# Kernel optimization log

Hardware: AMD Instinct MI355X
Metric: run time of the kernel (lower is better)

Reference implementation:

```python
import jax, jax.numpy as jnp
import numpy as np

LN_EPS = 1e-3  # Keras LayerNormalization default epsilon
EPS = 1e-8     # slot-attention weight epsilon
NUM_ITERS = 3


def layer_norm(x, g, b):
    m = jnp.mean(x, axis=-1, keepdims=True)
    v = jnp.var(x, axis=-1, keepdims=True)
    return g * (x - m) * jax.lax.rsqrt(v + LN_EPS) + b


def gru_cell(x, h, Wx, Wh, b_in, b_rec):
    # Keras GRUCell (reset_after=True): separate input and recurrent biases
    gx = x @ Wx + b_in      # [K, 3D]
    gh = h @ Wh + b_rec     # [K, 3D]
    xz, xr, xh = jnp.split(gx, 3, axis=-1)
    hz, hr, hh = jnp.split(gh, 3, axis=-1)
    z = jax.nn.sigmoid(xz + hz)
    r = jax.nn.sigmoid(xr + hr)
    h_cand = jnp.tanh(xh + r * hh)
    return z * h + (1.0 - z) * h_cand


def setup_inputs() -> dict:
    key = jax.random.key(0)
    N, C, D, H, K = 262144, 64, 64, 128, 4
    ks = jax.random.split(key, 32)
    w = lambda k, s: (jax.random.normal(k, s, jnp.float32) * 0.02)
    inp = {
        "x": jax.random.normal(ks[0], (N, C), jnp.float32),
        "noise_fg": jax.random.normal(ks[1], (K - 1, D), jnp.float32),
        "noise_bg": jax.random.normal(ks[2], (1, D), jnp.float32),
        "ln_in_g": jnp.ones((C,), jnp.float32),
        "ln_in_b": jnp.zeros((C,), jnp.float32),
        "mu_fg": w(ks[3], (1, D)),
        "log_sigma_fg": w(ks[4], (1, D)),
        "mu_bg": w(ks[5], (1, D)),
        "log_sigma_bg": w(ks[6], (1, D)),
        "Wk": w(ks[7], (C, D)),
        "Wv": w(ks[8], (C, D)),
        "qfg_g": jnp.ones((D,), jnp.float32),
        "qfg_b": jnp.zeros((D,), jnp.float32),
        "Wq_fg": w(ks[9], (D, D)),
        "qbg_g": jnp.ones((D,), jnp.float32),
        "qbg_b": jnp.zeros((D,), jnp.float32),
        "Wq_bg": w(ks[10], (D, D)),
        "gru_fg_Wx": w(ks[11], (D, 3 * D)),
        "gru_fg_Wh": w(ks[12], (D, 3 * D)),
        "gru_fg_bin": jnp.zeros((3 * D,), jnp.float32),
        "gru_fg_brec": jnp.zeros((3 * D,), jnp.float32),
        "gru_bg_Wx": w(ks[13], (D, 3 * D)),
        "gru_bg_Wh": w(ks[14], (D, 3 * D)),
        "gru_bg_bin": jnp.zeros((3 * D,), jnp.float32),
        "gru_bg_brec": jnp.zeros((3 * D,), jnp.float32),
        "mfg_g": jnp.ones((D,), jnp.float32),
        "mfg_b": jnp.zeros((D,), jnp.float32),
        "mfg_W1": w(ks[15], (D, H)),
        "mfg_b1": jnp.zeros((H,), jnp.float32),
        "mfg_W2": w(ks[16], (H, D)),
        "mfg_b2": jnp.zeros((D,), jnp.float32),
        "mbg_g": jnp.ones((D,), jnp.float32),
        "mbg_b": jnp.zeros((D,), jnp.float32),
        "mbg_W1": w(ks[17], (D, H)),
        "mbg_b1": jnp.zeros((H,), jnp.float32),
        "mbg_W2": w(ks[18], (H, D)),
        "mbg_b2": jnp.zeros((D,), jnp.float32),
    }
    return inp


def reference(x, noise_fg, noise_bg, ln_in_g, ln_in_b, mu_fg, log_sigma_fg, mu_bg,
              log_sigma_bg, Wk, Wv, qfg_g, qfg_b, Wq_fg, qbg_g, qbg_b, Wq_bg,
              gru_fg_Wx, gru_fg_Wh, gru_fg_bin, gru_fg_brec,
              gru_bg_Wx, gru_bg_Wh, gru_bg_bin, gru_bg_brec,
              mfg_g, mfg_b, mfg_W1, mfg_b1, mfg_W2, mfg_b2,
              mbg_g, mbg_b, mbg_W1, mbg_b1, mbg_W2, mbg_b2):
    D = Wk.shape[1]
    scale = D ** (-0.5)
    x = layer_norm(x, ln_in_g, ln_in_b)
    k = x @ Wk  # [N, D]
    v = x @ Wv  # [N, D]
    slots_fg = mu_fg + jnp.exp(log_sigma_fg) * noise_fg  # [K-1, D]
    slots_bg = mu_bg + jnp.exp(log_sigma_bg) * noise_bg  # [1, D]
    attn = None
    for _ in range(NUM_ITERS):
        q_fg = layer_norm(slots_fg, qfg_g, qfg_b) @ Wq_fg * scale  # [K-1, D]
        q_bg = layer_norm(slots_bg, qbg_g, qbg_b) @ Wq_bg * scale  # [1, D]
        logits = jnp.concatenate([k @ q_bg.T, k @ q_fg.T], axis=-1)  # [N, K]
        attn = jax.nn.softmax(logits, axis=-1)  # competition over slots
        w_all = attn + EPS
        w_all = w_all / jnp.sum(w_all, axis=0, keepdims=True)  # normalize over N
        updates = w_all.T @ v  # [K, D]
        upd_bg, upd_fg = updates[:1], updates[1:]
        slots_bg = gru_cell(upd_bg, slots_bg, gru_bg_Wx, gru_bg_Wh, gru_bg_bin, gru_bg_brec)
        slots_fg = gru_cell(upd_fg, slots_fg, gru_fg_Wx, gru_fg_Wh, gru_fg_bin, gru_fg_brec)
        h_bg = jax.nn.relu(layer_norm(slots_bg, mbg_g, mbg_b) @ mbg_W1 + mbg_b1)
        slots_bg = slots_bg + h_bg @ mbg_W2 + mbg_b2
        h_fg = jax.nn.relu(layer_norm(slots_fg, mfg_g, mfg_b) @ mfg_W1 + mfg_b1)
        slots_fg = slots_fg + h_fg @ mfg_W2 + mfg_b2
    slots = jnp.concatenate([slots_bg, slots_fg], axis=0)  # [K, D]
    return slots, attn.T  # attn: [K, N]
```

## Files before the change

kernel.cpp:

```cpp
#include <hip/hip_runtime.h>
#include <hip/hip_bf16.h>

#define N_ROWS   262144
#define ATT_BLOCKS 512
#define CHUNKS   2
#define LN_EPS_F 1e-3f
#define EPS_W    1e-8f
#define NEPS_F   (262144.0f*1e-8f)

__device__ __forceinline__ float bf2f(unsigned u){ return __uint_as_float((u&0xffffu)<<16); }
__device__ __forceinline__ unsigned cvtpk(float lo, float hi){
  unsigned r;
  asm("v_cvt_pk_bf16_f32 %0, %1, %2" : "=v"(r) : "v"(lo), "v"(hi));
  return r;
}
__device__ __forceinline__ float wave_sum64(float v){
#pragma unroll
  for (int off=1; off<64; off<<=1) v += __shfl_xor(v, off);
  return v;
}

__global__ __launch_bounds__(256) void attn_pass_kernel(
    const float* __restrict__ x, uint* __restrict__ xhat,
    const float* __restrict__ ucoef, float* __restrict__ pT,
    float* __restrict__ attn_out, float* __restrict__ slots,
    const float* __restrict__ noise_fg, const float* __restrict__ noise_bg,
    const float* __restrict__ mu_fg, const float* __restrict__ ls_fg,
    const float* __restrict__ mu_bg, const float* __restrict__ ls_bg,
    const float* __restrict__ ln_g, const float* __restrict__ ln_b,
    const float* __restrict__ Wk,
    const float* __restrict__ qfg_g, const float* __restrict__ qfg_b, const float* __restrict__ Wq_fg,
    const float* __restrict__ qbg_g, const float* __restrict__ qbg_b, const float* __restrict__ Wq_bg,
    int first, int last)
{
  __shared__ __align__(16) ushort xs[64*256];
  __shared__ __align__(16) uint2 attn_s[256];
  __shared__ __align__(16) float qs[256];
  __shared__ float qc[4];
  __shared__ float l4[256], q4s[256];
  const int tid = threadIdx.x;
  const int w = tid>>6, ln = tid&63;
  const int lm = ln&15, lg = ln>>4;
  const int blk = blockIdx.x;

  if (first){
    const float h0 = (w==0) ? fmaf(expf(ls_bg[ln]), noise_bg[ln], mu_bg[ln])
                            : fmaf(expf(ls_fg[ln]), noise_fg[(w-1)*64+ln], mu_fg[ln]);
    if (blk == 0) slots[w*64+ln] = h0;
    const float m  = wave_sum64(h0) * (1.f/64.f);
    const float vr = wave_sum64((h0-m)*(h0-m)) * (1.f/64.f);
    const float rs = rsqrtf(vr + LN_EPS_F);
    l4[tid] = (w==0?qbg_g:qfg_g)[ln]*(h0-m)*rs + (w==0?qbg_b:qfg_b)[ln];
    __syncthreads();
    {
      const float* __restrict__ Wqj = (w==0) ? Wq_bg : Wq_fg;
      float acc = 0.f;
#pragma unroll
      for (int dd = 0; dd < 64; ++dd) acc = fmaf(l4[w*64+dd], Wqj[dd*64+ln], acc);
      q4s[tid] = acc * 0.125f;
    }
    __syncthreads();
    {
      float t = 0.f;
#pragma unroll
      for (int oo = 0; oo < 64; ++oo) t = fmaf(Wk[ln*64+oo], q4s[w*64+oo], t);
      qs[ln*4 + w] = ln_g[ln]*t;
      const float cc = wave_sum64(ln_b[ln]*t);
      if (ln == 0) qc[w] = cc;
    }
  } else {
    qs[tid] = ucoef[tid];
    if (tid < 4) qc[tid] = ucoef[256+tid];
  }
  __syncthreads();

  float n0=0.f,n1=0.f,n2=0.f,n3=0.f, vs=0.f;
  float cs0=0.f, cs1=0.f, cs2=0.f, cs3=0.f;

  auto compute_chunk = [&](int c){
    const size_t rg = (size_t)blk*(CHUNKS*256) + (size_t)c*256;
    const int lrow = w*64 + lm*4;
    float la[4][4] = {};
#pragma unroll
    for (int dd = 0; dd < 16; ++dd){
      const int d = lg*16 + dd;
      const uint2 kk = *(const uint2*)&xs[d*256 + (((lrow>>3) ^ ((d*5)&31))<<3) + (lrow&7)];
      const float e0 = bf2f(kk.x), e1 = bf2f(kk.x>>16);
      const float e2 = bf2f(kk.y), e3 = bf2f(kk.y>>16);
      const float4 q4 = *(const float4*)&qs[d*4];
#pragma unroll
      for (int s = 0; s < 4; ++s){
        const float qv = (s==0)?q4.x:(s==1)?q4.y:(s==2)?q4.z:q4.w;
        la[0][s] = fmaf(e0, qv, la[0][s]);
        la[1][s] = fmaf(e1, qv, la[1][s]);
        la[2][s] = fmaf(e2, qv, la[2][s]);
        la[3][s] = fmaf(e3, qv, la[3][s]);
      }
    }
#pragma unroll
    for (int r = 0; r < 4; ++r)
#pragma unroll
      for (int s = 0; s < 4; ++s){
        la[r][s] += __shfl_xor(la[r][s], 16);
        la[r][s] += __shfl_xor(la[r][s], 32);
        la[r][s] += qc[s];
      }
    float av[4][4];
#pragma unroll
    for (int r = 0; r < 4; ++r){
      const float mx = fmaxf(fmaxf(la[r][0],la[r][1]), fmaxf(la[r][2],la[r][3]));
      const float e0 = __expf(la[r][0]-mx), e1 = __expf(la[r][1]-mx);
      const float e2 = __expf(la[r][2]-mx), e3 = __expf(la[r][3]-mx);
      const float inv = 1.0f/((e0+e1)+(e2+e3));
      av[r][0]=e0*inv; av[r][1]=e1*inv; av[r][2]=e2*inv; av[r][3]=e3*inv;
      cs0 += av[r][0]; cs1 += av[r][1]; cs2 += av[r][2]; cs3 += av[r][3];
    }
    if (lg == 0){
#pragma unroll
      for (int r = 0; r < 4; ++r){
        uint2 pk;
        pk.x = cvtpk(av[r][0], av[r][1]);
        pk.y = cvtpk(av[r][2], av[r][3]);
        attn_s[lrow + r] = pk;
      }
      if (last){
#pragma unroll
        for (int s = 0; s < 4; ++s){
          float4 o; o.x=av[0][s]; o.y=av[1][s]; o.z=av[2][s]; o.w=av[3][s];
          *(float4*)&attn_out[(size_t)s*N_ROWS + rg + lrow] = o;
        }
      }
    }
#pragma unroll
    for (int rb = 0; rb < 8; ++rb){
      const int ch = w*8 + rb;
      const uint4 vv = *(const uint4*)&xs[ln*256 + ((ch ^ ((ln*5)&31))<<3)];
      const ushort* vp = (const ushort*)&vv;
#pragma unroll
      for (int k2 = 0; k2 < 8; ++k2){
        const uint2 au = attn_s[ch*8 + k2];
        const float b0 = bf2f(au.x), b1 = bf2f(au.x>>16);
        const float b2 = bf2f(au.y), b3 = bf2f(au.y>>16);
        const float vvv = bf2f((unsigned)vp[k2]);
        n0 = fmaf(b0, vvv, n0); n1 = fmaf(b1, vvv, n1);
        n2 = fmaf(b2, vvv, n2); n3 = fmaf(b3, vvv, n3);
        vs += vvv;
      }
    }
  };

  if (first){
    for (int c = 0; c < CHUNKS; ++c){
      const size_t rg = (size_t)blk*(CHUNKS*256) + (size_t)c*256;
#pragma unroll
      for (int mi = 0; mi < 4; ++mi){
        const int trow = w*64 + mi*16 + lm;
        const float* xr = &x[(rg + trow)*64 + lg*8];
        const float4 a0 = *(const float4*)xr;
        const float4 a1 = *(const float4*)(xr+4);
        const float4 b0 = *(const float4*)(xr+32);
        const float4 b1 = *(const float4*)(xr+36);
        float s1 = ((a0.x+a0.y)+(a0.z+a0.w)) + ((a1.x+a1.y)+(a1.z+a1.w))
                 + ((b0.x+b0.y)+(b0.z+b0.w)) + ((b1.x+b1.y)+(b1.z+b1.w));
        float s2 = a0.x*a0.x; s2=fmaf(a0.y,a0.y,s2); s2=fmaf(a0.z,a0.z,s2); s2=fmaf(a0.w,a0.w,s2);
        s2=fmaf(a1.x,a1.x,s2); s2=fmaf(a1.y,a1.y,s2); s2=fmaf(a1.z,a1.z,s2); s2=fmaf(a1.w,a1.w,s2);
        s2=fmaf(b0.x,b0.x,s2); s2=fmaf(b0.y,b0.y,s2); s2=fmaf(b0.z,b0.z,s2); s2=fmaf(b0.w,b0.w,s2);
        s2=fmaf(b1.x,b1.x,s2); s2=fmaf(b1.y,b1.y,s2); s2=fmaf(b1.z,b1.z,s2); s2=fmaf(b1.w,b1.w,s2);
        s1 += __shfl_xor(s1,16); s2 += __shfl_xor(s2,16);
        s1 += __shfl_xor(s1,32); s2 += __shfl_xor(s2,32);
        const float m  = s1*(1.0f/64.0f);
        const float rs = rsqrtf(s2*(1.0f/64.0f) - m*m + LN_EPS_F);
        const float nm = -m*rs;
        float xv[16];
        xv[0]=fmaf(a0.x,rs,nm); xv[1]=fmaf(a0.y,rs,nm); xv[2]=fmaf(a0.z,rs,nm); xv[3]=fmaf(a0.w,rs,nm);
        xv[4]=fmaf(a1.x,rs,nm); xv[5]=fmaf(a1.y,rs,nm); xv[6]=fmaf(a1.z,rs,nm); xv[7]=fmaf(a1.w,rs,nm);
        xv[8]=fmaf(b0.x,rs,nm); xv[9]=fmaf(b0.y,rs,nm); xv[10]=fmaf(b0.z,rs,nm); xv[11]=fmaf(b0.w,rs,nm);
        xv[12]=fmaf(b1.x,rs,nm); xv[13]=fmaf(b1.y,rs,nm); xv[14]=fmaf(b1.z,rs,nm); xv[15]=fmaf(b1.w,rs,nm);
        const int ch = trow>>3, rr2 = trow&7;
#pragma unroll
        for (int p = 0; p < 8; ++p){
          const int d = lg*8 + p;
          xs[d*256 + ((ch ^ ((d*5)&31))<<3) + rr2] = (ushort)cvtpk(xv[p], xv[p]);
        }
#pragma unroll
        for (int p = 0; p < 8; ++p){
          const int d = 32 + lg*8 + p;
          xs[d*256 + ((ch ^ ((d*5)&31))<<3) + rr2] = (ushort)cvtpk(xv[8+p], xv[8+p]);
        }
      }
      __syncthreads();
      const size_t tile = (size_t)(blk*CHUNKS + c);
#pragma unroll
      for (int k = 0; k < 8; ++k){
        const int i = k*256 + tid;
        *(uint4*)&xhat[tile*8192 + i*4] = *(const uint4*)&xs[i*8];
      }
      compute_chunk(c);
      __syncthreads();
    }
  } else {
    uint4 sv[8];
    {
      const size_t t0 = (size_t)blk*CHUNKS;
#pragma unroll
      for (int k = 0; k < 8; ++k){ const int i = k*256 + tid; sv[k] = *(const uint4*)&xhat[t0*8192 + i*4]; }
#pragma unroll
      for (int k = 0; k < 8; ++k){ const int i = k*256 + tid; *(uint4*)&xs[i*8] = sv[k]; }
      __syncthreads();
    }
    for (int c = 0; c < CHUNKS; ++c){
      if (c+1 < CHUNKS){
        const size_t tl = (size_t)(blk*CHUNKS + c + 1);
#pragma unroll
        for (int k = 0; k < 8; ++k){ const int i = k*256 + tid; sv[k] = *(const uint4*)&xhat[tl*8192 + i*4]; }
      }
      compute_chunk(c);
      __syncthreads();
      if (c+1 < CHUNKS){
#pragma unroll
        for (int k = 0; k < 8; ++k){ const int i = k*256 + tid; *(uint4*)&xs[i*8] = sv[k]; }
        __syncthreads();
      }
    }
  }

  cs0 = wave_sum64(cs0)*0.25f; cs1 = wave_sum64(cs1)*0.25f;
  cs2 = wave_sum64(cs2)*0.25f; cs3 = wave_sum64(cs3)*0.25f;
  float* fp = (float*)xs;
  fp[w*256 + 0*64 + ln] = n0;
  fp[w*256 + 1*64 + ln] = n1;
  fp[w*256 + 2*64 + ln] = n2;
  fp[w*256 + 3*64 + ln] = n3;
  fp[1024 + w*64 + ln] = vs;
  if (ln == 0){ fp[1280+w*4+0]=cs0; fp[1280+w*4+1]=cs1; fp[1280+w*4+2]=cs2; fp[1280+w*4+3]=cs3; }
  __syncthreads();
  float* pb = pT + (size_t)blk*324;
  pb[tid] = fp[tid] + fp[256+tid] + fp[512+tid] + fp[768+tid];
  if (tid < 64)
    pb[256 + tid] = fp[1024+tid] + fp[1088+tid] + fp[1152+tid] + fp[1216+tid];
  if (tid < 4)
    pb[320 + tid] = fp[1280+tid] + fp[1284+tid] + fp[1288+tid] + fp[1292+tid];
}

__global__ __launch_bounds__(512) void update_kernel(int mode,
    const float* __restrict__ pT,
    float* __restrict__ slots, float* __restrict__ ucoef, float* __restrict__ out,
    const float* __restrict__ ln_g, const float* __restrict__ ln_b,
    const float* __restrict__ Wk, const float* __restrict__ Wv,
    const float* __restrict__ qfg_g, const float* __restrict__ qfg_b, const float* __restrict__ Wq_fg,
    const float* __restrict__ qbg_g, const float* __restrict__ qbg_b, const float* __restrict__ Wq_bg,
    const float* __restrict__ gfWx, const float* __restrict__ gfWh,
    const float* __restrict__ gfbin, const float* __restrict__ gfbrec,
    const float* __restrict__ gbWx, const float* __restrict__ gbWh,
    const float* __restrict__ gbbin, const float* __restrict__ gbbrec,
    const float* __restrict__ mfg_g, const float* __restrict__ mfg_b,
    const float* __restrict__ mfW1, const float* __restrict__ mfb1,
    const float* __restrict__ mfW2, const float* __restrict__ mfb2,
    const float* __restrict__ mbg_g, const float* __restrict__ mbg_b,
    const float* __restrict__ mbW1, const float* __restrict__ mbb1,
    const float* __restrict__ mbW2, const float* __restrict__ mbb2)
{
  const int j = blockIdx.x;
  const int tid = threadIdx.x;
  const int ln = tid & 63, wv = tid >> 6;
  const bool bg = (j == 0);

  __shared__ __align__(16) float wlds[24640];
  __shared__ float bi_s[192], br_s[192], b1_s[128], b2_s[64];
  __shared__ float mg_s[64], mbv_s[64], qg_s[64], qb_s[64], gl_s[64], bl_s[64];
  __shared__ float vin_s[64], u_s[64], h_s[64], hg_s[64], l_s[64], h1_s[128], ql_s[64];
  __shared__ float gxp[2][192], ghp[2][192];
  __shared__ float pn_s[8][64], pv_s[8][64], csw[8];
  __shared__ float p4[4][128], p8[8][64];

  const float* __restrict__ Wx = bg?gbWx:gfWx;  const float* __restrict__ Wh = bg?gbWh:gfWh;
  const float* __restrict__ bi = bg?gbbin:gfbin; const float* __restrict__ br = bg?gbbrec:gfbrec;
  const float* __restrict__ W1 = bg?mbW1:mfW1;  const float* __restrict__ b1 = bg?mbb1:mfb1;
  const float* __restrict__ W2 = bg?mbW2:mfW2;  const float* __restrict__ b2 = bg?mbb2:mfb2;
  const float* __restrict__ Wq = bg?Wq_bg:Wq_fg;

  float hnew = 0.f;

  if (tid < 192){ bi_s[tid] = bi[tid]; br_s[tid] = br[tid]; }
  else if (tid < 320){ const int i2 = tid-192; b1_s[i2] = b1[i2]; }
  else if (tid < 384){ const int i2 = tid-320; b2_s[i2] = b2[i2]; }
  else if (tid < 448){ const int i2 = tid-384; mg_s[i2] = (bg?mbg_g:mfg_g)[i2]; mbv_s[i2] = (bg?mbg_b:mfg_b)[i2]; }
  else               { const int i2 = tid-448; qg_s[i2] = (bg?qbg_g:qfg_g)[i2]; qb_s[i2] = (bg?qbg_b:qfg_b)[i2]; }
  if (tid < 64){ gl_s[tid] = ln_g[tid]; bl_s[tid] = ln_b[tid]; }
  { const float4* sA = (const float4*)Wx; const float4* sB = (const float4*)Wh;
    float4* dA = (float4*)wlds; float4* dB = (float4*)(wlds + 12288);
#pragma unroll
    for (int i = 0; i < 6; ++i){ dA[tid + i*512] = sA[tid + i*512]; dB[tid + i*512] = sB[tid + i*512]; } }

  {
    float a0 = 0.f, a1 = 0.f, a2 = 0.f;
    float c0 = 0.f, c1v = 0.f, c2v = 0.f;
    for (int bb = 0; bb < ATT_BLOCKS/8; bb += 16){
#pragma unroll
      for (int u = 0; u < 16; u += 2){
        const float* pa = pT + (size_t)((bb+u  )*8 + wv)*324;
        const float* pc = pT + (size_t)((bb+u+1)*8 + wv)*324;
        a0 += pa[j*64 + ln];  a1 += pa[256 + ln];  a2 += pa[320 + j];
        c0 += pc[j*64 + ln];  c1v += pc[256 + ln]; c2v += pc[320 + j];
      }
    }
    pn_s[wv][ln] = a0 + c0; pv_s[wv][ln] = a1 + c1v;
    if (ln == 0) csw[wv] = a2 + c2v;
  }
  if (tid < 64) h_s[tid] = slots[j*64 + tid];
  __syncthreads();
  if (tid < 64) {
    const float csum = ((csw[0]+csw[1])+(csw[2]+csw[3])) + ((csw[4]+csw[5])+(csw[6]+csw[7])) + NEPS_F;
    float nm = 0.f, vm = 0.f;
#pragma unroll
    for (int p2 = 0; p2 < 8; ++p2){ nm += pn_s[p2][tid]; vm += pv_s[p2][tid]; }
    vin_s[tid] = gl_s[tid]*(nm + EPS_W*vm)/csum + bl_s[tid];
  }
  __syncthreads();
  { const int p8i = tid >> 6;
    float a = 0.f;
    float wbuf[8];
#pragma unroll
    for (int dd = 0; dd < 8; ++dd) wbuf[dd] = Wv[(p8i*8+dd)*64 + ln];
#pragma unroll
    for (int dd = 0; dd < 8; ++dd) a = fmaf(vin_s[p8i*8+dd], wbuf[dd], a);
    p8[p8i][ln] = a;
  }
  __syncthreads();
  if (tid < 64)
    u_s[tid] = ((p8[0][tid]+p8[1][tid])+(p8[2][tid]+p8[3][tid]))
             + ((p8[4][tid]+p8[5][tid])+(p8[6][tid]+p8[7][tid]));
  __syncthreads();
  if (tid < 384) {
    const int gcol = tid % 192, gp = tid / 192;
    float ax = 0.f, ah = 0.f;
#pragma unroll
    for (int dd = 0; dd < 32; ++dd) {
      ax = fmaf(u_s[gp*32+dd], wlds[(gp*32+dd)*192 + gcol], ax);
      ah = fmaf(h_s[gp*32+dd], wlds[12288 + (gp*32+dd)*192 + gcol], ah);
    }
    gxp[gp][gcol] = ax; ghp[gp][gcol] = ah;
  }
  __syncthreads();
  { const float4* s1 = (const float4*)W1; const float4* s2 = (const float4*)W2; const float4* s3 = (const float4*)Wq;
    float4* d1 = (float4*)wlds; float4* d2 = (float4*)(wlds + 8192); float4* d3 = (float4*)(wlds + 16384);
#pragma unroll
    for (int i = 0; i < 4; ++i){ d1[tid + i*512] = s1[tid + i*512]; d2[tid + i*512] = s2[tid + i*512]; }
#pragma unroll
    for (int i = 0; i < 2; ++i){ d3[tid + i*512] = s3[tid + i*512]; }
#pragma unroll
    for (int k = 0; k < 8; ++k){
      const int i = tid + k*512;
      wlds[20480 + (i&63)*65 + (i>>6)] = Wk[i];
    } }
  if (tid < 64) {
    const float gx0 = gxp[0][tid]     + gxp[1][tid]     + bi_s[tid];
    const float gh0 = ghp[0][tid]     + ghp[1][tid]     + br_s[tid];
    const float gx1 = gxp[0][64+tid]  + gxp[1][64+tid]  + bi_s[64+tid];
    const float gh1 = ghp[0][64+tid]  + ghp[1][64+tid]  + br_s[64+tid];
    const float gx2 = gxp[0][128+tid] + gxp[1][128+tid] + bi_s[128+tid];
    const float gh2 = ghp[0][128+tid] + ghp[1][128+tid] + br_s[128+tid];
    const float h  = h_s[tid];
    const float z  = 1.f/(1.f + expf(-(gx0 + gh0)));
    const float rr = 1.f/(1.f + expf(-(gx1 + gh1)));
    const float hc = tanhf(gx2 + rr*gh2);
    const float hg = z*h + (1.f - z)*hc;
    hg_s[tid] = hg;
    const float m  = wave_sum64(hg) * (1.f/64.f);
    const float vr = wave_sum64((hg-m)*(hg-m)) * (1.f/64.f);
    const float rs = rsqrtf(vr + LN_EPS_F);
    l_s[tid] = mg_s[tid]*(hg-m)*rs + mbv_s[tid];
  }
  __syncthreads();
  { const int p4i = tid >> 7, hi = tid & 127;
    float a = 0.f;
#pragma unroll
    for (int dd = 0; dd < 16; ++dd) a = fmaf(l_s[p4i*16+dd], wlds[(p4i*16+dd)*128 + hi], a);
    p4[p4i][hi] = a;
  }
  __syncthreads();
  if (tid < 128) h1_s[tid] = fmaxf(((p4[0][tid]+p4[1][tid])+(p4[2][tid]+p4[3][tid])) + b1_s[tid], 0.f);
  __syncthreads();
  { const int p8i = tid >> 6;
    float a = 0.f;
#pragma unroll
    for (int dd = 0; dd < 16; ++dd) a = fmaf(h1_s[p8i*16+dd], wlds[8192 + (p8i*16+dd)*64 + ln], a);
    p8[p8i][ln] = a;
  }
  __syncthreads();
  if (tid < 64) {
    hnew = hg_s[tid] + b2_s[tid]
         + ((p8[0][tid]+p8[1][tid])+(p8[2][tid]+p8[3][tid]))
         + ((p8[4][tid]+p8[5][tid])+(p8[6][tid]+p8[7][tid]));
    slots[j*64 + tid] = hnew;
  }

  if (mode == 3) {
    if (tid < 64) out[j*64 + tid] = hnew;
  } else {
    if (tid < 64) {
      const float m  = wave_sum64(hnew) * (1.f/64.f);
      const float vr = wave_sum64((hnew-m)*(hnew-m)) * (1.f/64.f);
      const float rs = rsqrtf(vr + LN_EPS_F);
      l_s[tid] = qg_s[tid]*(hnew-m)*rs + qb_s[tid];
    }
    __syncthreads();
    { const int p8i = tid >> 6;
      float a = 0.f;
#pragma unroll
      for (int dd = 0; dd < 8; ++dd) a = fmaf(l_s[p8i*8+dd], wlds[16384 + (p8i*8+dd)*64 + ln], a);
      p8[p8i][ln] = a;
    }
    __syncthreads();
    if (tid < 64)
      ql_s[tid] = (((p8[0][tid]+p8[1][tid])+(p8[2][tid]+p8[3][tid]))
                  +((p8[4][tid]+p8[5][tid])+(p8[6][tid]+p8[7][tid]))) * 0.125f;
    __syncthreads();
    if (tid < 256){
      const int d = tid & 63, pt = tid >> 6;
      float ts = 0.f;
#pragma unroll
      for (int oo = 0; oo < 16; ++oo){
        const int o = pt*16 + oo;
        ts = fmaf(wlds[20480 + o*65 + d], ql_s[o], ts);
      }
      p8[pt][d] = ts;
    }
    __syncthreads();
    if (tid < 64){
      const float t = (p8[0][tid]+p8[1][tid]) + (p8[2][tid]+p8[3][tid]);
      ucoef[tid*4 + j] = gl_s[tid]*t;
      const float c = wave_sum64(bl_s[tid]*t);
      if (tid == 0) ucoef[256 + j] = c;
    }
  }
}

extern "C" void kernel_launch(void* const* d_in, const int* in_sizes, int n_in,
                              void* d_out, int out_size, void* d_ws, size_t ws_size,
                              hipStream_t stream)
{
  const float* x        = (const float*)d_in[0];
  const float* noise_fg = (const float*)d_in[1];
  const float* noise_bg = (const float*)d_in[2];
  const float* ln_g     = (const float*)d_in[3];
  const float* ln_b     = (const float*)d_in[4];
  const float* mu_fg    = (const float*)d_in[5];
  const float* ls_fg    = (const float*)d_in[6];
  const float* mu_bg    = (const float*)d_in[7];
  const float* ls_bg    = (const float*)d_in[8];
  const float* Wk       = (const float*)d_in[9];
  const float* Wv       = (const float*)d_in[10];
  const float* qfg_g    = (const float*)d_in[11];
  const float* qfg_b    = (const float*)d_in[12];
  const float* Wq_fg    = (const float*)d_in[13];
  const float* qbg_g    = (const float*)d_in[14];
  const float* qbg_b    = (const float*)d_in[15];
  const float* Wq_bg    = (const float*)d_in[16];
  const float* gfWx     = (const float*)d_in[17];
  const float* gfWh     = (const float*)d_in[18];
  const float* gfbin    = (const float*)d_in[19];
  const float* gfbrec   = (const float*)d_in[20];
  const float* gbWx     = (const float*)d_in[21];
  const float* gbWh     = (const float*)d_in[22];
  const float* gbbin    = (const float*)d_in[23];
  const float* gbbrec   = (const float*)d_in[24];
  const float* mfg_g    = (const float*)d_in[25];
  const float* mfg_b    = (const float*)d_in[26];
  const float* mfW1     = (const float*)d_in[27];
  const float* mfb1     = (const float*)d_in[28];
  const float* mfW2     = (const float*)d_in[29];
  const float* mfb2     = (const float*)d_in[30];
  const float* mbg_g    = (const float*)d_in[31];
  const float* mbg_b    = (const float*)d_in[32];
  const float* mbW1     = (const float*)d_in[33];
  const float* mbb1     = (const float*)d_in[34];
  const float* mbW2     = (const float*)d_in[35];
  const float* mbb2     = (const float*)d_in[36];

  float* out = (float*)d_out;

  char* ws = (char*)d_ws;
  uint*  xhat  = (uint*)ws;
  float* fws   = (float*)(ws + (size_t)ATT_BLOCKS*CHUNKS*8192*4);
  float* slots = fws;
  float* ucoef = fws + 256;
  float* pT    = fws + 1024;
  float* attn_out = out + 256;

  auto launch_attn = [&](int first, int last){
    attn_pass_kernel<<<ATT_BLOCKS, 256, 0, stream>>>(x, xhat, ucoef, pT, attn_out, slots,
      noise_fg, noise_bg, mu_fg, ls_fg, mu_bg, ls_bg, ln_g, ln_b, Wk,
      qfg_g, qfg_b, Wq_fg, qbg_g, qbg_b, Wq_bg, first, last);
  };
  auto launch_update = [&](int mode){
    update_kernel<<<4, 512, 0, stream>>>(mode, pT, slots, ucoef, out,
      ln_g, ln_b, Wk, Wv,
      qfg_g, qfg_b, Wq_fg, qbg_g, qbg_b, Wq_bg,
      gfWx, gfWh, gfbin, gfbrec, gbWx, gbWh, gbbin, gbbrec,
      mfg_g, mfg_b, mfW1, mfb1, mfW2, mfb2,
      mbg_g, mbg_b, mbW1, mbb1, mbW2, mbb2);
  };

  launch_attn(1, 0);
  launch_update(1);
  launch_attn(0, 0);
  launch_update(2);
  launch_attn(0, 1);
  launch_update(3);
}
```

Baseline: 109.4 us.

## Fuse slot update into attention pass via last-block atomic tail reduction

Removes the separate update kernel. The last four blocks of each attention pass detect completion through an atomic counter, spin until every block has arrived, then each computes one slot's GRU/MLP update and the next query coefficients. This cuts three kernel launches and their gaps. In exchange the update reads weights straight from global memory instead of staging them in LDS, it adds a spin-wait, and it needs a memset of the counters on each call.

```diff
diff --git a/kernel.cpp b/kernel.cpp
--- a/kernel.cpp
+++ b/kernel.cpp
@@ -22,31 +22,44 @@
 
 __global__ __launch_bounds__(256) void attn_pass_kernel(
     const float* __restrict__ x, uint* __restrict__ xhat,
-    const float* __restrict__ ucoef, float* __restrict__ pT,
-    float* __restrict__ attn_out, float* __restrict__ slots,
+    float* __restrict__ ucoef, float* __restrict__ pT,
+    float* __restrict__ attn_out, float* __restrict__ slots, float* __restrict__ out_slots,
+    int* __restrict__ cnt,
     const float* __restrict__ noise_fg, const float* __restrict__ noise_bg,
     const float* __restrict__ mu_fg, const float* __restrict__ ls_fg,
     const float* __restrict__ mu_bg, const float* __restrict__ ls_bg,
     const float* __restrict__ ln_g, const float* __restrict__ ln_b,
-    const float* __restrict__ Wk,
+    const float* __restrict__ Wk, const float* __restrict__ Wv,
     const float* __restrict__ qfg_g, const float* __restrict__ qfg_b, const float* __restrict__ Wq_fg,
     const float* __restrict__ qbg_g, const float* __restrict__ qbg_b, const float* __restrict__ Wq_bg,
-    int first, int last)
+    const float* __restrict__ gfWx, const float* __restrict__ gfWh,
+    const float* __restrict__ gfbin, const float* __restrict__ gfbrec,
+    const float* __restrict__ gbWx, const float* __restrict__ gbWh,
+    const float* __restrict__ gbbin, const float* __restrict__ gbbrec,
+    const float* __restrict__ mfg_g, const float* __restrict__ mfg_b,
+    const float* __restrict__ mfW1, const float* __restrict__ mfb1,
+    const float* __restrict__ mfW2, const float* __restrict__ mfb2,
+    const float* __restrict__ mbg_g, const float* __restrict__ mbg_b,
+    const float* __restrict__ mbW1, const float* __restrict__ mbb1,
+    const float* __restrict__ mbW2, const float* __restrict__ mbb2,
+    int pass)
 {
   __shared__ __align__(16) ushort xs[64*256];
   __shared__ __align__(16) uint2 attn_s[256];
   __shared__ __align__(16) float qs[256];
   __shared__ float qc[4];
-  __shared__ float l4[256], q4s[256];
+  __shared__ float l4[256], q4s[256], slot0_s[256];
+  __shared__ int tailj_s;
   const int tid = threadIdx.x;
   const int w = tid>>6, ln = tid&63;
   const int lm = ln&15, lg = ln>>4;
   const int blk = blockIdx.x;
+  const int first = (pass == 0), last = (pass == 2);
 
   if (first){
     const float h0 = (w==0) ? fmaf(expf(ls_bg[ln]), noise_bg[ln], mu_bg[ln])
                             : fmaf(expf(ls_fg[ln]), noise_fg[(w-1)*64+ln], mu_fg[ln]);
-    if (blk == 0) slots[w*64+ln] = h0;
+    slot0_s[tid] = h0;
     const float m  = wave_sum64(h0) * (1.f/64.f);
     const float vr = wave_sum64((h0-m)*(h0-m)) * (1.f/64.f);
     const float rs = rsqrtf(vr + LN_EPS_F);
@@ -240,126 +253,116 @@
     pb[256 + tid] = fp[1024+tid] + fp[1088+tid] + fp[1152+tid] + fp[1216+tid];
   if (tid < 4)
     pb[320 + tid] = fp[1280+tid] + fp[1284+tid] + fp[1288+tid] + fp[1292+tid];
-}
-
-__global__ __launch_bounds__(512) void update_kernel(int mode,
-    const float* __restrict__ pT,
-    float* __restrict__ slots, float* __restrict__ ucoef, float* __restrict__ out,
-    const float* __restrict__ ln_g, const float* __restrict__ ln_b,
-    const float* __restrict__ Wk, const float* __restrict__ Wv,
-    const float* __restrict__ qfg_g, const float* __restrict__ qfg_b, const float* __restrict__ Wq_fg,
-    const float* __restrict__ qbg_g, const float* __restrict__ qbg_b, const float* __restrict__ Wq_bg,
-    const float* __restrict__ gfWx, const float* __restrict__ gfWh,
-    const float* __restrict__ gfbin, const float* __restrict__ gfbrec,
-    const float* __restrict__ gbWx, const float* __restrict__ gbWh,
-    const float* __restrict__ gbbin, const float* __restrict__ gbbrec,
-    const float* __restrict__ mfg_g, const float* __restrict__ mfg_b,
-    const float* __restrict__ mfW1, const float* __restrict__ mfb1,
-    const float* __restrict__ mfW2, const float* __restrict__ mfb2,
-    const float* __restrict__ mbg_g, const float* __restrict__ mbg_b,
-    const float* __restrict__ mbW1, const float* __restrict__ mbb1,
-    const float* __restrict__ mbW2, const float* __restrict__ mbb2)
-{
-  const int j = blockIdx.x;
-  const int tid = threadIdx.x;
-  const int ln = tid & 63, wv = tid >> 6;
-  const bool bg = (j == 0);
-
-  __shared__ __align__(16) float wlds[24640];
-  __shared__ float bi_s[192], br_s[192], b1_s[128], b2_s[64];
-  __shared__ float mg_s[64], mbv_s[64], qg_s[64], qb_s[64], gl_s[64], bl_s[64];
-  __shared__ float vin_s[64], u_s[64], h_s[64], hg_s[64], l_s[64], h1_s[128], ql_s[64];
-  __shared__ float gxp[2][192], ghp[2][192];
-  __shared__ float pn_s[8][64], pv_s[8][64], csw[8];
-  __shared__ float p4[4][128], p8[8][64];
-
-  const float* __restrict__ Wx = bg?gbWx:gfWx;  const float* __restrict__ Wh = bg?gbWh:gfWh;
-  const float* __restrict__ bi = bg?gbbin:gfbin; const float* __restrict__ br = bg?gbbrec:gfbrec;
-  const float* __restrict__ W1 = bg?mbW1:mfW1;  const float* __restrict__ b1 = bg?mbb1:mfb1;
-  const float* __restrict__ W2 = bg?mbW2:mfW2;  const float* __restrict__ b2 = bg?mbb2:mfb2;
-  const float* __restrict__ Wq = bg?Wq_bg:Wq_fg;
-
-  float hnew = 0.f;
-
-  if (tid < 192){ bi_s[tid] = bi[tid]; br_s[tid] = br[tid]; }
-  else if (tid < 320){ const int i2 = tid-192; b1_s[i2] = b1[i2]; }
-  else if (tid < 384){ const int i2 = tid-320; b2_s[i2] = b2[i2]; }
-  else if (tid < 448){ const int i2 = tid-384; mg_s[i2] = (bg?mbg_g:mfg_g)[i2]; mbv_s[i2] = (bg?mbg_b:mfg_b)[i2]; }
-  else               { const int i2 = tid-448; qg_s[i2] = (bg?qbg_g:qfg_g)[i2]; qb_s[i2] = (bg?qbg_b:qfg_b)[i2]; }
-  if (tid < 64){ gl_s[tid] = ln_g[tid]; bl_s[tid] = ln_b[tid]; }
-  { const float4* sA = (const float4*)Wx; const float4* sB = (const float4*)Wh;
-    float4* dA = (float4*)wlds; float4* dB = (float4*)(wlds + 12288);
-#pragma unroll
-    for (int i = 0; i < 6; ++i){ dA[tid + i*512] = sA[tid + i*512]; dB[tid + i*512] = sB[tid + i*512]; } }
+
+  __threadfence();
+  if (tid == 0){
+    const int old = atomicAdd(&cnt[pass], 1);
+    tailj_s = (old >= ATT_BLOCKS-4) ? (old - (ATT_BLOCKS-4)) : -1;
+  }
+  __syncthreads();
+  const int tj = tailj_s;
+  if (tj < 0) return;
+  if (tid == 0){ while (atomicAdd(&cnt[pass], 0) < ATT_BLOCKS) {} }
+  __syncthreads();
+  __threadfence();
+
+  const bool bg = (tj == 0);
+  const float* __restrict__ Wxp = bg?gbWx:gfWx;  const float* __restrict__ Whp = bg?gbWh:gfWh;
+  const float* __restrict__ bip = bg?gbbin:gfbin; const float* __restrict__ brp = bg?gbbrec:gfbrec;
+  const float* __restrict__ W1p = bg?mbW1:mfW1;  const float* __restrict__ b1p = bg?mbb1:mfb1;
+  const float* __restrict__ W2p = bg?mbW2:mfW2;  const float* __restrict__ b2p = bg?mbb2:mfb2;
+  const float* __restrict__ Wqp = bg?Wq_bg:Wq_fg;
+  const float* __restrict__ Wvp = Wv;
+
+  float* fx = (float*)xs;
+  float* pn4 = fx;
+  float* pv4 = fx + 256;
+  float* cs4 = fx + 512;
+  float* vin_s = fx + 520;
+  float* u_s   = fx + 584;
+  float* h_s   = fx + 648;
+  float* gx_s  = fx + 720;
+  float* gh_s  = fx + 912;
+  float* hg_s  = fx + 1104;
+  float* l_s2  = fx + 1168;
+  float* h1_s  = fx + 1232;
+  float* pu    = fx + 1360;
+  float* pm    = fx + 1616;
+  float* ql2   = fx + 1872;
 
   {
-    float a0 = 0.f, a1 = 0.f, a2 = 0.f;
-    float c0 = 0.f, c1v = 0.f, c2v = 0.f;
-    for (int bb = 0; bb < ATT_BLOCKS/8; bb += 16){
+    float a0=0,a1=0,a2=0, c0=0,c1=0,c2=0;
+    for (int bb = 0; bb < ATT_BLOCKS/4; bb += 16){
 #pragma unroll
       for (int u = 0; u < 16; u += 2){
-        const float* pa = pT + (size_t)((bb+u  )*8 + wv)*324;
-        const float* pc = pT + (size_t)((bb+u+1)*8 + wv)*324;
-        a0 += pa[j*64 + ln];  a1 += pa[256 + ln];  a2 += pa[320 + j];
-        c0 += pc[j*64 + ln];  c1v += pc[256 + ln]; c2v += pc[320 + j];
-      }
-    }
-    pn_s[wv][ln] = a0 + c0; pv_s[wv][ln] = a1 + c1v;
-    if (ln == 0) csw[wv] = a2 + c2v;
-  }
-  if (tid < 64) h_s[tid] = slots[j*64 + tid];
-  __syncthreads();
-  if (tid < 64) {
-    const float csum = ((csw[0]+csw[1])+(csw[2]+csw[3])) + ((csw[4]+csw[5])+(csw[6]+csw[7])) + NEPS_F;
+        const float* pa = pT + (size_t)((bb+u  )*4 + w)*324;
+        const float* pc = pT + (size_t)((bb+u+1)*4 + w)*324;
+        a0 += pa[tj*64+ln]; a1 += pa[256+ln]; a2 += pa[320+tj];
+        c0 += pc[tj*64+ln]; c1 += pc[256+ln]; c2 += pc[320+tj];
+      }
+    }
+    pn4[w*64+ln] = a0+c0; pv4[w*64+ln] = a1+c1;
+    if (ln == 0) cs4[w] = a2+c2;
+  }
+  __syncthreads();
+  if (tid < 64){
+    const float csum = (cs4[0]+cs4[1])+(cs4[2]+cs4[3]) + NEPS_F;
     float nm = 0.f, vm = 0.f;
 #pragma unroll
-    for (int p2 = 0; p2 < 8; ++p2){ nm += pn_s[p2][tid]; vm += pv_s[p2][tid]; }
-    vin_s[tid] = gl_s[tid]*(nm + EPS_W*vm)/csum + bl_s[tid];
-  }
-  __syncthreads();
-  { const int p8i = tid >> 6;
+    for (int p = 0; p < 4; ++p){ nm += pn4[p*64+tid]; vm += pv4[p*64+tid]; }
+    vin_s[tid] = ln_g[tid]*(nm + EPS_W*vm)/csum + ln_b[tid];
+    h_s[tid] = first ? slot0_s[tj*64+tid] : slots[tj*64+tid];
+  }
+  __syncthreads();
+  {
+    float wb[16];
+#pragma unroll
+    for (int dd=0; dd<16; ++dd) wb[dd] = Wvp[(w*16+dd)*64 + ln];
     float a = 0.f;
-    float wbuf[8];
-#pragma unroll
-    for (int dd = 0; dd < 8; ++dd) wbuf[dd] = Wv[(p8i*8+dd)*64 + ln];
-#pragma unroll
-    for (int dd = 0; dd < 8; ++dd) a = fmaf(vin_s[p8i*8+dd], wbuf[dd], a);
-    p8[p8i][ln] = a;
-  }
-  __syncthreads();
-  if (tid < 64)
-    u_s[tid] = ((p8[0][tid]+p8[1][tid])+(p8[2][tid]+p8[3][tid]))
-             + ((p8[4][tid]+p8[5][tid])+(p8[6][tid]+p8[7][tid]));
-  __syncthreads();
-  if (tid < 384) {
-    const int gcol = tid % 192, gp = tid / 192;
-    float ax = 0.f, ah = 0.f;
-#pragma unroll
-    for (int dd = 0; dd < 32; ++dd) {
-      ax = fmaf(u_s[gp*32+dd], wlds[(gp*32+dd)*192 + gcol], ax);
-      ah = fmaf(h_s[gp*32+dd], wlds[12288 + (gp*32+dd)*192 + gcol], ah);
-    }
-    gxp[gp][gcol] = ax; ghp[gp][gcol] = ah;
-  }
-  __syncthreads();
-  { const float4* s1 = (const float4*)W1; const float4* s2 = (const float4*)W2; const float4* s3 = (const float4*)Wq;
-    float4* d1 = (float4*)wlds; float4* d2 = (float4*)(wlds + 8192); float4* d3 = (float4*)(wlds + 16384);
-#pragma unroll
-    for (int i = 0; i < 4; ++i){ d1[tid + i*512] = s1[tid + i*512]; d2[tid + i*512] = s2[tid + i*512]; }
-#pragma unroll
-    for (int i = 0; i < 2; ++i){ d3[tid + i*512] = s3[tid + i*512]; }
-#pragma unroll
-    for (int k = 0; k < 8; ++k){
-      const int i = tid + k*512;
-      wlds[20480 + (i&63)*65 + (i>>6)] = Wk[i];
-    } }
-  if (tid < 64) {
-    const float gx0 = gxp[0][tid]     + gxp[1][tid]     + bi_s[tid];
-    const float gh0 = ghp[0][tid]     + ghp[1][tid]     + br_s[tid];
-    const float gx1 = gxp[0][64+tid]  + gxp[1][64+tid]  + bi_s[64+tid];
-    const float gh1 = ghp[0][64+tid]  + ghp[1][64+tid]  + br_s[64+tid];
-    const float gx2 = gxp[0][128+tid] + gxp[1][128+tid] + bi_s[128+tid];
-    const float gh2 = ghp[0][128+tid] + ghp[1][128+tid] + br_s[128+tid];
+#pragma unroll
+    for (int dd=0; dd<16; ++dd) a = fmaf(vin_s[w*16+dd], wb[dd], a);
+    pu[w*64+ln] = a;
+  }
+  __syncthreads();
+  if (tid < 64) u_s[tid] = (pu[tid]+pu[64+tid])+(pu[128+tid]+pu[192+tid]);
+  __syncthreads();
+  {
+    const int m0 = (tid < 192) ? 0 : 1;
+    const int c0i = (tid < 192) ? tid : (tid - 192);
+    const float* __restrict__ Wm = m0 ? Whp : Wxp;
+    const float* vsrc = m0 ? h_s : u_s;
+    float acc = 0.f;
+#pragma unroll
+    for (int c8 = 0; c8 < 4; ++c8){
+      float wr[16];
+#pragma unroll
+      for (int u2=0; u2<16; ++u2) wr[u2] = Wm[(c8*16+u2)*192 + c0i];
+#pragma unroll
+      for (int u2=0; u2<16; ++u2) acc = fmaf(vsrc[c8*16+u2], wr[u2], acc);
+    }
+    if (m0) gh_s[c0i] = acc; else gx_s[c0i] = acc;
+  }
+  if (tid < 128){
+    const int c1i = 64 + tid;
+    float acc = 0.f;
+#pragma unroll
+    for (int c8 = 0; c8 < 4; ++c8){
+      float wr[16];
+#pragma unroll
+      for (int u2=0; u2<16; ++u2) wr[u2] = Whp[(c8*16+u2)*192 + c1i];
+#pragma unroll
+      for (int u2=0; u2<16; ++u2) acc = fmaf(h_s[c8*16+u2], wr[u2], acc);
+    }
+    gh_s[c1i] = acc;
+  }
+  __syncthreads();
+  if (tid < 64){
+    const float gx0 = gx_s[tid]     + bip[tid];
+    const float gh0 = gh_s[tid]     + brp[tid];
+    const float gx1 = gx_s[64+tid]  + bip[64+tid];
+    const float gh1 = gh_s[64+tid]  + brp[64+tid];
+    const float gx2 = gx_s[128+tid] + bip[128+tid];
+    const float gh2 = gh_s[128+tid] + brp[128+tid];
     const float h  = h_s[tid];
     const float z  = 1.f/(1.f + expf(-(gx0 + gh0)));
     const float rr = 1.f/(1.f + expf(-(gx1 + gh1)));
@@ -369,69 +372,79 @@
     const float m  = wave_sum64(hg) * (1.f/64.f);
     const float vr = wave_sum64((hg-m)*(hg-m)) * (1.f/64.f);
     const float rs = rsqrtf(vr + LN_EPS_F);
-    l_s[tid] = mg_s[tid]*(hg-m)*rs + mbv_s[tid];
-  }
-  __syncthreads();
-  { const int p4i = tid >> 7, hi = tid & 127;
+    l_s2[tid] = (bg?mbg_g:mfg_g)[tid]*(hg-m)*rs + (bg?mbg_b:mfg_b)[tid];
+  }
+  __syncthreads();
+  {
+    const int hi = tid & 127, pt = tid >> 7;
     float a = 0.f;
 #pragma unroll
-    for (int dd = 0; dd < 16; ++dd) a = fmaf(l_s[p4i*16+dd], wlds[(p4i*16+dd)*128 + hi], a);
-    p4[p4i][hi] = a;
-  }
-  __syncthreads();
-  if (tid < 128) h1_s[tid] = fmaxf(((p4[0][tid]+p4[1][tid])+(p4[2][tid]+p4[3][tid])) + b1_s[tid], 0.f);
-  __syncthreads();
-  { const int p8i = tid >> 6;
+    for (int c8 = 0; c8 < 2; ++c8){
+      float wr[16];
+#pragma unroll
+      for (int u2=0; u2<16; ++u2) wr[u2] = W1p[(pt*32+c8*16+u2)*128 + hi];
+#pragma unroll
+      for (int u2=0; u2<16; ++u2) a = fmaf(l_s2[pt*32+c8*16+u2], wr[u2], a);
+    }
+    pm[pt*128+hi] = a;
+  }
+  __syncthreads();
+  if (tid < 128) h1_s[tid] = fmaxf(pm[tid] + pm[128+tid] + b1p[tid], 0.f);
+  __syncthreads();
+  {
     float a = 0.f;
 #pragma unroll
-    for (int dd = 0; dd < 16; ++dd) a = fmaf(h1_s[p8i*16+dd], wlds[8192 + (p8i*16+dd)*64 + ln], a);
-    p8[p8i][ln] = a;
-  }
-  __syncthreads();
-  if (tid < 64) {
-    hnew = hg_s[tid] + b2_s[tid]
-         + ((p8[0][tid]+p8[1][tid])+(p8[2][tid]+p8[3][tid]))
-         + ((p8[4][tid]+p8[5][tid])+(p8[6][tid]+p8[7][tid]));
-    slots[j*64 + tid] = hnew;
-  }
-
-  if (mode == 3) {
-    if (tid < 64) out[j*64 + tid] = hnew;
-  } else {
-    if (tid < 64) {
+    for (int c8 = 0; c8 < 2; ++c8){
+      float wr[16];
+#pragma unroll
+      for (int u2=0; u2<16; ++u2) wr[u2] = W2p[(w*32+c8*16+u2)*64 + ln];
+#pragma unroll
+      for (int u2=0; u2<16; ++u2) a = fmaf(h1_s[w*32+c8*16+u2], wr[u2], a);
+    }
+    pu[w*64+ln] = a;
+  }
+  __syncthreads();
+  float hnew = 0.f;
+  if (tid < 64){
+    hnew = hg_s[tid] + b2p[tid] + (pu[tid]+pu[64+tid])+(pu[128+tid]+pu[192+tid]);
+    slots[tj*64 + tid] = hnew;
+    if (last) out_slots[tj*64 + tid] = hnew;
+  }
+  if (!last){
+    if (tid < 64){
       const float m  = wave_sum64(hnew) * (1.f/64.f);
       const float vr = wave_sum64((hnew-m)*(hnew-m)) * (1.f/64.f);
       const float rs = rsqrtf(vr + LN_EPS_F);
-      l_s[tid] = qg_s[tid]*(hnew-m)*rs + qb_s[tid];
+      l_s2[tid] = (bg?qbg_g:qfg_g)[tid]*(hnew-m)*rs + (bg?qbg_b:qfg_b)[tid];
     }
     __syncthreads();
-    { const int p8i = tid >> 6;
+    {
       float a = 0.f;
-#pragma unroll
-      for (int dd = 0; dd < 8; ++dd) a = fmaf(l_s[p8i*8+dd], wlds[16384 + (p8i*8+dd)*64 + ln], a);
-      p8[p8i][ln] = a;
+      float wr[16];
+#pragma unroll
+      for (int dd=0; dd<16; ++dd) wr[dd] = Wqp[(w*16+dd)*64 + ln];
+#pragma unroll
+      for (int dd=0; dd<16; ++dd) a = fmaf(l_s2[w*16+dd], wr[dd], a);
+      pu[w*64+ln] = a;
     }
     __syncthreads();
-    if (tid < 64)
-      ql_s[tid] = (((p8[0][tid]+p8[1][tid])+(p8[2][tid]+p8[3][tid]))
-                  +((p8[4][tid]+p8[5][tid])+(p8[6][tid]+p8[7][tid]))) * 0.125f;
+    if (tid < 64) ql2[tid] = ((pu[tid]+pu[64+tid])+(pu[128+tid]+pu[192+tid])) * 0.125f;
     __syncthreads();
-    if (tid < 256){
-      const int d = tid & 63, pt = tid >> 6;
-      float ts = 0.f;
-#pragma unroll
-      for (int oo = 0; oo < 16; ++oo){
-        const int o = pt*16 + oo;
-        ts = fmaf(wlds[20480 + o*65 + d], ql_s[o], ts);
-      }
-      p8[pt][d] = ts;
+    {
+      float a = 0.f;
+      float wr[16];
+#pragma unroll
+      for (int oo=0; oo<16; ++oo) wr[oo] = Wk[ln*64 + w*16 + oo];
+#pragma unroll
+      for (int oo=0; oo<16; ++oo) a = fmaf(ql2[w*16+oo], wr[oo], a);
+      pu[w*64+ln] = a;
     }
     __syncthreads();
     if (tid < 64){
-      const float t = (p8[0][tid]+p8[1][tid]) + (p8[2][tid]+p8[3][tid]);
-      ucoef[tid*4 + j] = gl_s[tid]*t;
-      const float c = wave_sum64(bl_s[tid]*t);
-      if (tid == 0) ucoef[256 + j] = c;
+      const float t2 = (pu[tid]+pu[64+tid])+(pu[128+tid]+pu[192+tid]);
+      ucoef[tid*4 + tj] = ln_g[tid]*t2;
+      const float cc = wave_sum64(ln_b[tid]*t2);
+      if (tid == 0) ucoef[256 + tj] = cc;
     }
   }
 }
@@ -486,26 +499,18 @@
   float* slots = fws;
   float* ucoef = fws + 256;
   float* pT    = fws + 1024;
+  int*   cnt   = (int*)(pT + (size_t)ATT_BLOCKS*324);
   float* attn_out = out + 256;
 
-  auto launch_attn = [&](int first, int last){
-    attn_pass_kernel<<<ATT_BLOCKS, 256, 0, stream>>>(x, xhat, ucoef, pT, attn_out, slots,
-      noise_fg, noise_bg, mu_fg, ls_fg, mu_bg, ls_bg, ln_g, ln_b, Wk,
-      qfg_g, qfg_b, Wq_fg, qbg_g, qbg_b, Wq_bg, first, last);
-  };
-  auto launch_update = [&](int mode){
-    update_kernel<<<4, 512, 0, stream>>>(mode, pT, slots, ucoef, out,
-      ln_g, ln_b, Wk, Wv,
+  hipMemsetAsync(cnt, 0, 16, stream);
+
+  for (int pass = 0; pass < 3; ++pass){
+    attn_pass_kernel<<<ATT_BLOCKS, 256, 0, stream>>>(x, xhat, ucoef, pT, attn_out,
+      slots, out, cnt,
+      noise_fg, noise_bg, mu_fg, ls_fg, mu_bg, ls_bg, ln_g, ln_b, Wk, Wv,
       qfg_g, qfg_b, Wq_fg, qbg_g, qbg_b, Wq_bg,
       gfWx, gfWh, gfbin, gfbrec, gbWx, gbWh, gbbin, gbbrec,
       mfg_g, mfg_b, mfW1, mfb1, mfW2, mfb2,
-      mbg_g, mbg_b, mbW1, mbb1, mbW2, mbb2);
-  };
-
-  launch_attn(1, 0);
-  launch_update(1);
-  launch_attn(0, 0);
-  launch_update(2);
-  launch_attn(0, 1);
-  launch_update(3);
+      mbg_g, mbg_b, mbW1, mbb1, mbW2, mbb2, pass);
+  }
 }
```

New measurement: 221.6 us. +102.6%, slower.
